# Kernel optimization log

Hardware: AMD Instinct MI355X
Metric: run time of the kernel (lower is better)

The kernel has to match this reference:

```python
import jax, jax.numpy as jnp
import numpy as np

D = 512

def _resmlp(x, W1, W2):
    # residual MLP: x + silu(x W1) W2  (e3nn-style bias-free linears)
    return x + jax.nn.silu(x @ W1) @ W2

def setup_inputs() -> dict:
    key = jax.random.key(0)
    ks = jax.random.split(key, 12)
    s = 1.0 / np.sqrt(D)
    mk = lambda k: jax.random.normal(k, (D, D), dtype=jnp.float32) * s
    return {
        "x": jax.random.normal(ks[0], (4, 4096, D), dtype=jnp.float32),
        "qW1": mk(ks[1]), "qW2": mk(ks[2]),
        "kW1": mk(ks[3]), "kW2": mk(ks[4]),
        "vW1": mk(ks[5]), "vW2": mk(ks[6]),
        "aWq": mk(ks[7]), "aWk": mk(ks[8]), "aWv": mk(ks[9]),
        "Wout": mk(ks[10]),
    }

def reference(x, qW1, qW2, kW1, kW2, vW1, vW2, aWq, aWk, aWv, Wout):
    # ResiMLP q/k/v projections on node features [B, N, D]
    q = _resmlp(x, qW1, qW2) @ aWq
    k = _resmlp(x, kW1, kW2) @ aWk
    v = _resmlp(x, vW1, vW2) @ aWv
    # naive full attention: bmm -> softmax(dim=1, over QUERY axis) -> bmm
    attn = jnp.einsum("bqd,bkd->bqk", q, k)   # [B, Nq, Nk]
    attn = jax.nn.softmax(attn, axis=1)        # faithful to Softmax(dim=1)
    out = jnp.einsum("bqk,bkd->bqd", attn, v)  # [B, N, D]
    return out @ Wout
```

## Files before the change

### kernel.cpp

```cpp
#include <hip/hip_runtime.h>
#include <hip/hip_bf16.h>
#include <stdint.h>
#include <stddef.h>

typedef _Float16 f16;
typedef __attribute__((ext_vector_type(8))) _Float16 f16x8;
typedef __attribute__((ext_vector_type(4))) float f32x4;

#define EPI_NONE 0
#define EPI_SILU 1
#define EPI_RES  2
#define OUT_F16    0
#define OUT_F32    1
#define OUT_VT     3
#define OUT_ESTATS 4

__device__ __forceinline__ void gll16(const f16* g, char* l) {
    __builtin_amdgcn_global_load_lds(
        (const __attribute__((address_space(1))) void*)g,
        (__attribute__((address_space(3))) void*)l, 16, 0, 0);
}

template<int BN, int EPI, int OUT, int AEC>
__global__ __launch_bounds__(256)
void gemm_f16(const f16* __restrict__ A, const f16* __restrict__ Bm,
              void* __restrict__ Cp, const float* __restrict__ Res,
              float* __restrict__ mp, float* __restrict__ zp,
              const float* __restrict__ cScale,
              int kseg, int lda, int ldb, int ldc, int ldr,
              unsigned long long sA, unsigned long long sB, unsigned long long sC)
{
    constexpr int NWF = BN / 32;

    const f16* Ag = A + (size_t)blockIdx.z * sA;
    const f16* Bg = Bm + (size_t)blockIdx.z * sB;
    const size_t zC = (size_t)blockIdx.z * sC;

    unsigned nwg = gridDim.x * gridDim.y;
    unsigned lin = blockIdx.y * gridDim.x + blockIdx.x;
    unsigned cpx = nwg >> 3;
    unsigned swz = (lin & 7) * cpx + (lin >> 3);
    unsigned bxs = swz % gridDim.x, bys = swz / gridDim.x;

    const int t    = threadIdx.x;
    const int w    = t >> 6;
    const int lane = t & 63;
    const int wr   = w >> 1, wc = w & 1;
    const int lo   = lane & 15, hi = lane >> 4;
    const int brow = bys * 128;
    const int bcol = bxs * BN;

    __shared__ f16 As[128 * 64];
    __shared__ f16 Bs[BN * 64];
    __shared__ float smst[(OUT == OUT_ESTATS) ? 512 : 4];

    f32x4 acc[4][NWF];
#pragma unroll
    for (int m = 0; m < 4; ++m)
#pragma unroll
        for (int n = 0; n < NWF; ++n)
            acc[m][n] = (f32x4){0.f, 0.f, 0.f, 0.f};

    const int r0 = t >> 3;
    const int cswz = ((t & 7) ^ ((t >> 3) & 7)) * 8;
    const int rA7  = lo & 7;

    const float* cb = nullptr;
    f16x8 bq[NWF];
    float4 cq0, cq1;
    if constexpr (AEC) {
        cb = cScale + ((size_t)blockIdx.z * 32 + (brow >> 7)) * 4096;
#pragma unroll
        for (int i = 0; i < NWF; ++i)
            bq[i] = *(const f16x8*)(Bg + (size_t)(bcol + i * 32 + r0) * ldb + cswz);
        cq0 = *(const float4*)(cb + cswz);
        cq1 = *(const float4*)(cb + cswz + 4);
    }

    for (int k0 = 0; k0 < kseg; k0 += 64) {
#pragma unroll
        for (int i = 0; i < 4; ++i)
            gll16(Ag + (size_t)(brow + i * 32 + r0) * lda + (k0 + cswz),
                  (char*)As + i * 4096 + w * 1024);
        if constexpr (AEC) {
            float cf[8] = {cq0.x, cq0.y, cq0.z, cq0.w, cq1.x, cq1.y, cq1.z, cq1.w};
#pragma unroll
            for (int i = 0; i < NWF; ++i) {
                f16x8 ev = bq[i], pv;
#pragma unroll
                for (int j = 0; j < 8; ++j) pv[j] = (f16)((float)ev[j] * cf[j]);
                *(f16x8*)((char*)Bs + i * 4096 + t * 16) = pv;
            }
            if (k0 + 64 < kseg) {
#pragma unroll
                for (int i = 0; i < NWF; ++i)
                    bq[i] = *(const f16x8*)(Bg + (size_t)(bcol + i * 32 + r0) * ldb
                                            + (k0 + 64 + cswz));
                cq0 = *(const float4*)(cb + k0 + 64 + cswz);
                cq1 = *(const float4*)(cb + k0 + 64 + cswz + 4);
            }
        } else {
#pragma unroll
            for (int i = 0; i < NWF; ++i)
                gll16(Bg + (size_t)(bcol + i * 32 + r0) * ldb + (k0 + cswz),
                      (char*)Bs + i * 4096 + w * 1024);
        }
        __syncthreads();

#pragma unroll
        for (int kk = 0; kk < 64; kk += 32) {
            f16x8 aH[4], bH[NWF];
#pragma unroll
            for (int m = 0; m < 4; ++m) {
                int idx = (wr * 64 + m * 16 + lo) * 64 +
                          ((((kk >> 3) + hi) ^ rA7) * 8);
                aH[m] = *(const f16x8*)&As[idx];
            }
#pragma unroll
            for (int n = 0; n < NWF; ++n) {
                int idx = (wc * (BN / 2) + n * 16 + lo) * 64 +
                          ((((kk >> 3) + hi) ^ rA7) * 8);
                bH[n] = *(const f16x8*)&Bs[idx];
            }
#pragma unroll
            for (int m = 0; m < 4; ++m)
#pragma unroll
                for (int n = 0; n < NWF; ++n)
                    acc[m][n] = __builtin_amdgcn_mfma_f32_16x16x32_f16(
                        aH[m], bH[n], acc[m][n], 0, 0, 0);
        }
        __syncthreads();
    }

    if constexpr (OUT == OUT_ESTATS) {
        const size_t zS = (size_t)blockIdx.z * (32 * 4096);
        float mb[NWF];
#pragma unroll
        for (int n = 0; n < NWF; ++n) {
            float ml = acc[0][n][0];
#pragma unroll
            for (int m = 0; m < 4; ++m)
#pragma unroll
                for (int j = 0; j < 4; ++j) ml = fmaxf(ml, acc[m][n][j]);
            ml = fmaxf(ml, __shfl_xor(ml, 16));
            ml = fmaxf(ml, __shfl_xor(ml, 32));
            if (hi == 0) smst[wr * 128 + wc * (BN / 2) + n * 16 + lo] = ml;
        }
        __syncthreads();
#pragma unroll
        for (int n = 0; n < NWF; ++n) {
            int c = wc * (BN / 2) + n * 16 + lo;
            mb[n] = fmaxf(smst[c], smst[128 + c]);
        }
        float zsum[NWF];
#pragma unroll
        for (int n = 0; n < NWF; ++n) {
            zsum[n] = 0.f;
            int col = bcol + wc * (BN / 2) + n * 16 + lo;
#pragma unroll
            for (int m = 0; m < 4; ++m)
#pragma unroll
                for (int j = 0; j < 4; ++j) {
                    int row = brow + wr * 64 + m * 16 + hi * 4 + j;
                    float e = __expf(acc[m][n][j] - mb[n]);
                    zsum[n] += e;
                    ((f16*)Cp)[(size_t)row * ldc + col + zC] = (f16)e;
                }
        }
        __syncthreads();
#pragma unroll
        for (int n = 0; n < NWF; ++n) {
            float zl = zsum[n];
            zl += __shfl_xor(zl, 16);
            zl += __shfl_xor(zl, 32);
            if (hi == 0) smst[256 + wr * 128 + wc * (BN / 2) + n * 16 + lo] = zl;
        }
        __syncthreads();
        if (t < 128) {
            float m0 = smst[t],       m1 = smst[128 + t];
            float z0 = smst[256 + t], z1 = smst[384 + t];
            size_t o = zS + (size_t)(brow >> 7) * 4096 + bcol + t;
            mp[o] = fmaxf(m0, m1);
            zp[o] = z0 + z1;
        }
        return;
    }

#pragma unroll
    for (int m = 0; m < 4; ++m) {
#pragma unroll
        for (int n = 0; n < NWF; ++n) {
            if constexpr (OUT == OUT_VT) {
                int row0 = brow + wr * 64 + m * 16 + hi * 4;
                int col  = bcol + wc * (BN / 2) + n * 16 + lo;
                int bb = row0 >> 12, n0 = row0 & 4095;
                unsigned short u[4];
#pragma unroll
                for (int j = 0; j < 4; ++j) {
                    f16 vb = (f16)acc[m][n][j];
                    u[j] = *(unsigned short*)&vb;
                }
                ushort4 pack = {u[0], u[1], u[2], u[3]};
                *(ushort4*)&((f16*)Cp)[((size_t)(bb * 512 + col) << 12) + n0] = pack;
            } else {
#pragma unroll
                for (int j = 0; j < 4; ++j) {
                    int row = brow + wr * 64 + m * 16 + hi * 4 + j;
                    int col = bcol + wc * (BN / 2) + n * 16 + lo;
                    size_t idx = (size_t)row * ldc + col + zC;
                    float v = acc[m][n][j];
                    if (EPI == EPI_SILU) v = v / (1.f + __expf(-v));
                    if (EPI == EPI_RES)  v += Res[(size_t)row * ldr + col];
                    if (OUT == OUT_F32) ((float*)Cp)[idx] = v;
                    else                ((f16*)Cp)[idx] = (f16)v;
                }
            }
        }
    }
}

__global__ void cast_x_kernel(const float* __restrict__ x, f16* __restrict__ xf)
{
    size_t i = ((size_t)blockIdx.x * 256 + threadIdx.x) * 8;
    float4 a = *(const float4*)(x + i);
    float4 b = *(const float4*)(x + i + 4);
    f16x8 o;
    o[0] = (f16)a.x; o[1] = (f16)a.y; o[2] = (f16)a.z; o[3] = (f16)a.w;
    o[4] = (f16)b.x; o[5] = (f16)b.y; o[6] = (f16)b.z; o[7] = (f16)b.w;
    *(f16x8*)(xf + i) = o;
}

struct WPack { const float* W[10]; f16* H[10]; };

__global__ void transw_all_kernel(WPack p)
{
    const float* W = p.W[blockIdx.z];
    f16* WT = p.H[blockIdx.z];
    __shared__ float tile[32][33];
    int bx = blockIdx.x * 32, by = blockIdx.y * 32;
    int tx = threadIdx.x, ty = threadIdx.y;
#pragma unroll
    for (int i = 0; i < 32; i += 8)
        tile[ty + i][tx] = W[(size_t)(by + ty + i) * 512 + bx + tx];
    __syncthreads();
#pragma unroll
    for (int i = 0; i < 32; i += 8)
        WT[(size_t)(bx + ty + i) * 512 + by + tx] = (f16)tile[tx][ty + i];
}

__global__ void colstats_comb_kernel(const float* __restrict__ mp,
                                     const float* __restrict__ zp,
                                     float* __restrict__ cB)
{
    size_t base = (size_t)blockIdx.y * (32 * 4096);
    int col = blockIdx.x * 256 + threadIdx.x;
    float m = -1e30f;
#pragma unroll
    for (int i = 0; i < 32; ++i) m = fmaxf(m, mp[base + i * 4096 + col]);
    float z = 0.f;
#pragma unroll
    for (int i = 0; i < 32; ++i)
        z += zp[base + i * 4096 + col] * __expf(mp[base + i * 4096 + col] - m);
    float r = 1.f / z;
#pragma unroll
    for (int i = 0; i < 32; ++i)
        cB[base + i * 4096 + col] = __expf(mp[base + i * 4096 + col] - m) * r;
}

extern "C" void kernel_launch(void* const* d_in, const int* in_sizes, int n_in,
                              void* d_out, int out_size, void* d_ws, size_t ws_size,
                              hipStream_t stream)
{
    const int B = 4, N = 4096, D = 512;
    const size_t MALL = (size_t)B * N;
    const size_t ND = MALL * D;
    const size_t NN = (size_t)N * N;
    const size_t WW = (size_t)D * D;
    const float* x = (const float*)d_in[0];
    const float* Wf[10];
    for (int i = 0; i < 10; ++i) Wf[i] = (const float*)d_in[1 + i];

    char* ws = (char*)d_ws;
    size_t off = 0;
    auto carve = [&](size_t bytes) -> char* {
        char* p = ws + off;
        off = (off + bytes + 255) & ~(size_t)255;
        return p;
    };

    const size_t PLANE = NN * 2;
    f16* E_all = (f16*)carve(4 * PLANE);
    f16* QKf   = (f16*)carve(PLANE);
    f16* VT    = (f16*)carve((size_t)B * D * N * 2);
    f16* O     = (f16*)carve(ND * 2);
    f16* wc1   = (f16*)carve(3 * WW * 2);
    f16* wc2   = (f16*)carve(3 * WW * 2);
    f16* wcA   = (f16*)carve(2 * WW * 2);
    f16* wv3   = (f16*)carve(WW * 2);
    f16* wo    = (f16*)carve(WW * 2);
    float* mp  = (float*)carve((size_t)B * 32 * 4096 * 4);
    float* zp  = (float*)carve((size_t)B * 32 * 4096 * 4);
    float* cB  = (float*)carve((size_t)B * 32 * 4096 * 4);

    f16* xf = E_all;
    f16* t1 = E_all + ND;
    f16* h  = t1 + MALL * 1536;
    (void)in_sizes; (void)n_in; (void)out_size; (void)ws_size;

    cast_x_kernel<<<dim3((unsigned)(ND / 2048)), 256, 0, stream>>>(x, xf);
    WPack wp;
    wp.W[0] = Wf[0]; wp.H[0] = wc1;
    wp.W[1] = Wf[2]; wp.H[1] = wc1 + WW;
    wp.W[2] = Wf[4]; wp.H[2] = wc1 + 2 * WW;
    wp.W[3] = Wf[1]; wp.H[3] = wc2;
    wp.W[4] = Wf[3]; wp.H[4] = wc2 + WW;
    wp.W[5] = Wf[5]; wp.H[5] = wc2 + 2 * WW;
    wp.W[6] = Wf[6]; wp.H[6] = wcA;
    wp.W[7] = Wf[7]; wp.H[7] = wcA + WW;
    wp.W[8] = Wf[8]; wp.H[8] = wv3;
    wp.W[9] = Wf[9]; wp.H[9] = wo;
    transw_all_kernel<<<dim3(16, 16, 10), dim3(32, 8), 0, stream>>>(wp);

    gemm_f16<128, EPI_SILU, OUT_F16, 0><<<dim3(12, 128), 256, 0, stream>>>(
        xf, wc1, t1, nullptr, nullptr, nullptr, nullptr,
        512, 512, 512, 1536, 512, 0, 0, 0);
    gemm_f16<128, EPI_RES, OUT_F16, 0><<<dim3(4, 128, 3), 256, 0, stream>>>(
        t1, wc2, h, x, nullptr, nullptr, nullptr,
        512, 1536, 512, 1536, 512, 512, WW, 512);
    gemm_f16<128, EPI_NONE, OUT_F16, 0><<<dim3(4, 128, 2), 256, 0, stream>>>(
        h, wcA, QKf, nullptr, nullptr, nullptr, nullptr,
        512, 1536, 512, 1024, 512, 512, WW, 512);
    gemm_f16<128, EPI_NONE, OUT_VT, 0><<<dim3(4, 128), 256, 0, stream>>>(
        h + 1024, wv3, VT, nullptr, nullptr, nullptr, nullptr,
        512, 1536, 512, 512, 512, 0, 0, 0);

    gemm_f16<128, EPI_NONE, OUT_ESTATS, 0><<<dim3(32, 32, 4), 256, 0, stream>>>(
        QKf, QKf + 512, E_all, nullptr, mp, zp, nullptr,
        512, 1024, 1024, 4096, 4096,
        (unsigned long long)N * 1024, (unsigned long long)N * 1024, NN);
    colstats_comb_kernel<<<dim3(16, 4), 256, 0, stream>>>(mp, zp, cB);

    gemm_f16<64, EPI_NONE, OUT_F16, 1><<<dim3(8, 32, 4), 256, 0, stream>>>(
        E_all, VT, O, nullptr, nullptr, nullptr, cB,
        4096, 4096, 4096, 512, 512,
        NN, (unsigned long long)D * N, (unsigned long long)N * D);

    gemm_f16<128, EPI_NONE, OUT_F32, 0><<<dim3(4, 128), 256, 0, stream>>>(
        O, wo, d_out, nullptr, nullptr, nullptr, nullptr,
        512, 512, 512, 512, 512, 0, 0, 0);
}
```

Before: 377.3 us.

## Fuse Q/K/V projection GEMMs, add 2D tile swizzle, alias LDS, nontemporal E stores

The Q, K and V attention projection GEMMs are merged into one launch over a concatenated weight buffer. Each block picks its A-slice from its column range and writes either row-major QK or transposed V. The scores GEMM gets a fixed 2D block swizzle to improve L2 reuse of Q/K tiles. The exp-score stores become nontemporal, and shared memory is unified into one aliased buffer so the stats scratch reuses tile space, which may raise occupancy. The risks are a hardcoded 32x32 grid in the swizzle and cache-policy effects on the E matrix, which is read back by the next GEMM.

```diff
diff --git a/kernel.cpp b/kernel.cpp
--- a/kernel.cpp
+++ b/kernel.cpp
@@ -14,6 +14,7 @@
 #define OUT_F32    1
 #define OUT_VT     3
 #define OUT_ESTATS 4
+#define OUT_QKV    5
 
 __device__ __forceinline__ void gll16(const f16* g, char* l) {
     __builtin_amdgcn_global_load_lds(
@@ -21,10 +22,11 @@
         (__attribute__((address_space(3))) void*)l, 16, 0, 0);
 }
 
-template<int BN, int EPI, int OUT, int AEC>
+template<int BN, int EPI, int OUT, int AEC, int SWZ2D>
 __global__ __launch_bounds__(256)
 void gemm_f16(const f16* __restrict__ A, const f16* __restrict__ Bm,
-              void* __restrict__ Cp, const float* __restrict__ Res,
+              void* __restrict__ Cp, f16* __restrict__ Cp2,
+              const float* __restrict__ Res,
               float* __restrict__ mp, float* __restrict__ zp,
               const float* __restrict__ cScale,
               int kseg, int lda, int ldb, int ldc, int ldr,
@@ -32,15 +34,21 @@
 {
     constexpr int NWF = BN / 32;
 
-    const f16* Ag = A + (size_t)blockIdx.z * sA;
-    const f16* Bg = Bm + (size_t)blockIdx.z * sB;
     const size_t zC = (size_t)blockIdx.z * sC;
 
-    unsigned nwg = gridDim.x * gridDim.y;
-    unsigned lin = blockIdx.y * gridDim.x + blockIdx.x;
-    unsigned cpx = nwg >> 3;
-    unsigned swz = (lin & 7) * cpx + (lin >> 3);
-    unsigned bxs = swz % gridDim.x, bys = swz / gridDim.x;
+    unsigned bxs, bys;
+    if constexpr (SWZ2D) {
+        unsigned lin = blockIdx.y * 32 + blockIdx.x;
+        unsigned c = lin & 7, idx = lin >> 3;
+        bys = (c >> 2) * 16 + (idx >> 3);
+        bxs = (c & 3) * 8 + (idx & 7);
+    } else {
+        unsigned nwg = gridDim.x * gridDim.y;
+        unsigned lin = blockIdx.y * gridDim.x + blockIdx.x;
+        unsigned cpx = nwg >> 3;
+        unsigned swz = (lin & 7) * cpx + (lin >> 3);
+        bxs = swz % gridDim.x; bys = swz / gridDim.x;
+    }
 
     const int t    = threadIdx.x;
     const int w    = t >> 6;
@@ -50,9 +58,14 @@
     const int brow = bys * 128;
     const int bcol = bxs * BN;
 
-    __shared__ f16 As[128 * 64];
-    __shared__ f16 Bs[BN * 64];
-    __shared__ float smst[(OUT == OUT_ESTATS) ? 512 : 4];
+    const f16* Ag = A + (size_t)blockIdx.z * sA;
+    const f16* Bg = Bm + (size_t)blockIdx.z * sB;
+    if constexpr (OUT == OUT_QKV) Ag += (size_t)(bcol >> 9) * 512;
+
+    __shared__ __align__(16) char ldsbuf[16384 + BN * 128];
+    f16* As = (f16*)ldsbuf;
+    f16* Bs = (f16*)(ldsbuf + 16384);
+    float* smst = (float*)ldsbuf;
 
     f32x4 acc[4][NWF];
 #pragma unroll
@@ -164,7 +177,8 @@
                     int row = brow + wr * 64 + m * 16 + hi * 4 + j;
                     float e = __expf(acc[m][n][j] - mb[n]);
                     zsum[n] += e;
-                    ((f16*)Cp)[(size_t)row * ldc + col + zC] = (f16)e;
+                    __builtin_nontemporal_store(
+                        (f16)e, &((f16*)Cp)[(size_t)row * ldc + col + zC]);
                 }
         }
         __syncthreads();
@@ -202,6 +216,27 @@
                 }
                 ushort4 pack = {u[0], u[1], u[2], u[3]};
                 *(ushort4*)&((f16*)Cp)[((size_t)(bb * 512 + col) << 12) + n0] = pack;
+            } else if constexpr (OUT == OUT_QKV) {
+                if (bcol < 1024) {
+#pragma unroll
+                    for (int j = 0; j < 4; ++j) {
+                        int row = brow + wr * 64 + m * 16 + hi * 4 + j;
+                        int col = bcol + wc * (BN / 2) + n * 16 + lo;
+                        ((f16*)Cp)[(size_t)row * 1024 + col] = (f16)acc[m][n][j];
+                    }
+                } else {
+                    int row0 = brow + wr * 64 + m * 16 + hi * 4;
+                    int col  = bcol + wc * (BN / 2) + n * 16 + lo - 1024;
+                    int bb = row0 >> 12, n0 = row0 & 4095;
+                    unsigned short u[4];
+#pragma unroll
+                    for (int j = 0; j < 4; ++j) {
+                        f16 vb = (f16)acc[m][n][j];
+                        u[j] = *(unsigned short*)&vb;
+                    }
+                    ushort4 pack = {u[0], u[1], u[2], u[3]};
+                    *(ushort4*)&Cp2[((size_t)(bb * 512 + col) << 12) + n0] = pack;
+                }
             } else {
 #pragma unroll
                 for (int j = 0; j < 4; ++j) {
@@ -295,8 +330,7 @@
     f16* O     = (f16*)carve(ND * 2);
     f16* wc1   = (f16*)carve(3 * WW * 2);
     f16* wc2   = (f16*)carve(3 * WW * 2);
-    f16* wcA   = (f16*)carve(2 * WW * 2);
-    f16* wv3   = (f16*)carve(WW * 2);
+    f16* wcA   = (f16*)carve(3 * WW * 2);
     f16* wo    = (f16*)carve(WW * 2);
     float* mp  = (float*)carve((size_t)B * 32 * 4096 * 4);
     float* zp  = (float*)carve((size_t)B * 32 * 4096 * 4);
@@ -317,35 +351,32 @@
     wp.W[5] = Wf[5]; wp.H[5] = wc2 + 2 * WW;
     wp.W[6] = Wf[6]; wp.H[6] = wcA;
     wp.W[7] = Wf[7]; wp.H[7] = wcA + WW;
-    wp.W[8] = Wf[8]; wp.H[8] = wv3;
+    wp.W[8] = Wf[8]; wp.H[8] = wcA + 2 * WW;
     wp.W[9] = Wf[9]; wp.H[9] = wo;
     transw_all_kernel<<<dim3(16, 16, 10), dim3(32, 8), 0, stream>>>(wp);
 
-    gemm_f16<128, EPI_SILU, OUT_F16, 0><<<dim3(12, 128), 256, 0, stream>>>(
-        xf, wc1, t1, nullptr, nullptr, nullptr, nullptr,
+    gemm_f16<128, EPI_SILU, OUT_F16, 0, 0><<<dim3(12, 128), 256, 0, stream>>>(
+        xf, wc1, t1, nullptr, nullptr, nullptr, nullptr, nullptr,
         512, 512, 512, 1536, 512, 0, 0, 0);
-    gemm_f16<128, EPI_RES, OUT_F16, 0><<<dim3(4, 128, 3), 256, 0, stream>>>(
-        t1, wc2, h, x, nullptr, nullptr, nullptr,
+    gemm_f16<128, EPI_RES, OUT_F16, 0, 0><<<dim3(4, 128, 3), 256, 0, stream>>>(
+        t1, wc2, h, nullptr, x, nullptr, nullptr, nullptr,
         512, 1536, 512, 1536, 512, 512, WW, 512);
-    gemm_f16<128, EPI_NONE, OUT_F16, 0><<<dim3(4, 128, 2), 256, 0, stream>>>(
-        h, wcA, QKf, nullptr, nullptr, nullptr, nullptr,
-        512, 1536, 512, 1024, 512, 512, WW, 512);
-    gemm_f16<128, EPI_NONE, OUT_VT, 0><<<dim3(4, 128), 256, 0, stream>>>(
-        h + 1024, wv3, VT, nullptr, nullptr, nullptr, nullptr,
-        512, 1536, 512, 512, 512, 0, 0, 0);
-
-    gemm_f16<128, EPI_NONE, OUT_ESTATS, 0><<<dim3(32, 32, 4), 256, 0, stream>>>(
-        QKf, QKf + 512, E_all, nullptr, mp, zp, nullptr,
+    gemm_f16<128, EPI_NONE, OUT_QKV, 0, 0><<<dim3(12, 128), 256, 0, stream>>>(
+        h, wcA, QKf, VT, nullptr, nullptr, nullptr, nullptr,
+        512, 1536, 512, 1024, 512, 0, 0, 0);
+
+    gemm_f16<128, EPI_NONE, OUT_ESTATS, 0, 1><<<dim3(32, 32, 4), 256, 0, stream>>>(
+        QKf, QKf + 512, E_all, nullptr, nullptr, mp, zp, nullptr,
         512, 1024, 1024, 4096, 4096,
         (unsigned long long)N * 1024, (unsigned long long)N * 1024, NN);
     colstats_comb_kernel<<<dim3(16, 4), 256, 0, stream>>>(mp, zp, cB);
 
-    gemm_f16<64, EPI_NONE, OUT_F16, 1><<<dim3(8, 32, 4), 256, 0, stream>>>(
-        E_all, VT, O, nullptr, nullptr, nullptr, cB,
+    gemm_f16<64, EPI_NONE, OUT_F16, 1, 0><<<dim3(8, 32, 4), 256, 0, stream>>>(
+        E_all, VT, O, nullptr, nullptr, nullptr, nullptr, cB,
         4096, 4096, 4096, 512, 512,
         NN, (unsigned long long)D * N, (unsigned long long)N * D);
 
-    gemm_f16<128, EPI_NONE, OUT_F32, 0><<<dim3(4, 128), 256, 0, stream>>>(
-        O, wo, d_out, nullptr, nullptr, nullptr, nullptr,
+    gemm_f16<128, EPI_NONE, OUT_F32, 0, 0><<<dim3(4, 128), 256, 0, stream>>>(
+        O, wo, d_out, nullptr, nullptr, nullptr, nullptr, nullptr,
         512, 512, 512, 512, 512, 0, 0, 0);
 }
```

New measurement: 424.4 us. 12.5% more time.
